# Performance work log

Measured on AMD Instinct MI355X. Metric: run time of the kernel, lower is better.

## Reference

```python
import jax, jax.numpy as jnp
import numpy as np

VAR_CXCY = 0.1   # SSD encoding variances
VAR_WH = 0.2
THRESH = 0.5     # match threshold from forward()
EPS = 1e-6


def point_form(p):
    """[P,4] (cx,cy,w,h) -> (x1,y1,x2,y2)."""
    return jnp.concatenate([p[..., :2] - p[..., 2:] / 2,
                            p[..., :2] + p[..., 2:] / 2], axis=-1)


def iou(a, b):
    """a: [N,4] xyxy, b: [P,4] xyxy -> [N,P] jaccard overlap."""
    lt = jnp.maximum(a[:, None, :2], b[None, :, :2])
    rb = jnp.minimum(a[:, None, 2:], b[None, :, 2:])
    wh = jnp.clip(rb - lt, 0.0)
    inter = wh[..., 0] * wh[..., 1]
    area_a = (a[:, 2] - a[:, 0]) * (a[:, 3] - a[:, 1])
    area_b = (b[:, 2] - b[:, 0]) * (b[:, 3] - b[:, 1])
    return inter / (area_a[:, None] + area_b[None, :] - inter + EPS)


def match_one(gt, labels, priors, priors_pt):
    """SSD match for a single image.
    gt: [N,4] xyxy, labels: [N] int, priors: [P,4] cxcywh, priors_pt: [P,4] xyxy.
    Returns loc targets [P,4] and conf targets [P] (0 = background).
    """
    ov = iou(gt, priors_pt)                       # [N,P]
    best_prior_idx = jnp.argmax(ov, axis=1)        # [N] best prior per gt
    best_truth_ov = jnp.max(ov, axis=0)            # [P]
    best_truth_idx = jnp.argmax(ov, axis=0)        # [P] best gt per prior
    n = gt.shape[0]
    # ensure every gt keeps its best prior
    best_truth_ov = best_truth_ov.at[best_prior_idx].set(2.0)
    best_truth_idx = best_truth_idx.at[best_prior_idx].set(jnp.arange(n))
    matches = gt[best_truth_idx]                   # [P,4]
    conf = labels[best_truth_idx] + 1              # shift so 0 = background
    conf = jnp.where(best_truth_ov < THRESH, 0, conf)
    # encode matched boxes relative to priors
    m_cxcy = (matches[:, :2] + matches[:, 2:]) * 0.5
    m_wh = jnp.clip(matches[:, 2:] - matches[:, :2], EPS)
    g_cxcy = (m_cxcy - priors[:, :2]) / (VAR_CXCY * priors[:, 2:])
    g_wh = jnp.log(m_wh / priors[:, 2:]) / VAR_WH
    return jnp.concatenate([g_cxcy, g_wh], axis=1), conf


def setup_inputs() -> dict:
    key = jax.random.key(0)
    k1, k2, k3, k4, k5 = jax.random.split(key, 5)
    B, N, P = 32, 100, 8732
    # ground-truth boxes: valid xyxy corners in [0,1]
    xy1 = jax.random.uniform(k1, (B, N, 2)) * 0.7
    wh = 0.05 + jax.random.uniform(k2, (B, N, 2)) * 0.25
    gt_boxes = jnp.concatenate([xy1, xy1 + wh], axis=-1).astype(jnp.float32)
    gt_labels = jax.random.randint(k3, (B, N), 0, 20)
    # priors: cxcywh
    p_cxcy = jax.random.uniform(k4, (P, 2))
    p_wh = 0.05 + jax.random.uniform(k5, (P, 2)) * 0.45
    priors = jnp.concatenate([p_cxcy, p_wh], axis=-1).astype(jnp.float32)
    return {"gt_boxes": gt_boxes, "gt_labels": gt_labels, "priors": priors}


def reference(gt_boxes, gt_labels, priors):
    priors_pt = point_form(priors)
    loc_t, conf_t = jax.vmap(
        lambda g, l: match_one(g, l, priors, priors_pt))(gt_boxes, gt_labels)
    return loc_t, conf_t
```

## Files before the change

### kernel.cpp

```cpp
#include <hip/hip_runtime.h>

#pragma clang fp contract(off)

#define BB 32
#define NN 100
#define PP 8732
#define NBX 35

template <bool USE_PART>
__global__ __launch_bounds__(256) void k_iou_pass(
    const float* __restrict__ gt,
    const float* __restrict__ priors,
    unsigned long long* __restrict__ red,
    unsigned char* __restrict__ m8)
{
    __shared__ float s_area[NN];
    __shared__ unsigned long long s_part[NN][5];

    const int b = blockIdx.y;
    const int t = threadIdx.x;
    const int p = blockIdx.x * 256 + t;
    const bool valid = p < PP;
    const int pc = valid ? p : (PP - 1);

    const float4* __restrict__ gtb =
        reinterpret_cast<const float4*>(gt) + b * NN;

    if (t < NN) {
        float4 g = gtb[t];
        s_area[t] = (g.z - g.x) * (g.w - g.y);
    }

    const float4 pr = reinterpret_cast<const float4*>(priors)[pc];
    const float px1 = pr.x - pr.z * 0.5f;
    const float py1 = pr.y - pr.w * 0.5f;
    const float px2 = pr.x + pr.z * 0.5f;
    const float py2 = pr.y + pr.w * 0.5f;
    const float area_b = (px2 - px1) * (py2 - py1);

    float best_ov = -1.0f;
    int best_j = 0;

    const int wbase = blockIdx.x * 256 + (t & ~63);
    const int wid = t >> 6;
    const bool lane0 = (t & 63) == 0;

    __syncthreads();

    #pragma unroll 4
    for (int j = 0; j < NN; ++j) {
        float4 g = gtb[j];
        float area_a = s_area[j];
        float ltx = fmaxf(g.x, px1), lty = fmaxf(g.y, py1);
        float rbx = fminf(g.z, px2), rby = fminf(g.w, py2);
        float w = fmaxf(rbx - ltx, 0.0f), h = fmaxf(rby - lty, 0.0f);
        float inter = w * h;
        float iou = inter / (area_a + area_b - inter + 1e-6f);

        if (iou > best_ov) { best_ov = iou; best_j = j; }

        float m = iou;
        m = fmaxf(m, __shfl_xor(m, 1));
        m = fmaxf(m, __shfl_xor(m, 2));
        m = fmaxf(m, __shfl_xor(m, 4));
        m = fmaxf(m, __shfl_xor(m, 8));
        m = fmaxf(m, __shfl_xor(m, 16));
        m = fmaxf(m, __shfl_xor(m, 32));
        unsigned long long win = __ballot(iou == m);
        int lmin = __ffsll((long long)win) - 1;
        if (lane0) {
            s_part[j][wid] =
                ((unsigned long long)__float_as_uint(m) << 32) |
                (unsigned int)(~(wbase + lmin));
        }
    }
    __syncthreads();

    if (t < NN) {
        unsigned long long best = s_part[t][0];
        #pragma unroll
        for (int w = 1; w < 4; ++w) {
            unsigned long long k = s_part[t][w];
            if (k > best) best = k;
        }
        if (USE_PART) {
            red[((size_t)b * NBX + blockIdx.x) * NN + t] = best;
        } else {
            atomicMax(&red[b * NN + t], best);
        }
    }
    if (valid) {
        m8[b * PP + p] =
            (unsigned char)(best_j | ((best_ov < 0.5f) ? 0x80 : 0));
    }
}

template <bool USE_PART>
__global__ __launch_bounds__(256) void k_encode(
    const float* __restrict__ gt,
    const int*   __restrict__ labels,
    const float* __restrict__ priors,
    const unsigned long long* __restrict__ red,
    const unsigned char* __restrict__ m8,
    float* __restrict__ loc_out,
    float* __restrict__ conf_out)
{
    __shared__ int s_forced[256];

    const int b = blockIdx.y;
    const int t = threadIdx.x;
    const int p = blockIdx.x * 256 + t;

    s_forced[t] = -1;
    __syncthreads();
    if (t < NN) {
        unsigned long long best;
        if (USE_PART) {
            const unsigned long long* q = red + (size_t)b * NBX * NN + t;
            best = q[0];
            #pragma unroll 5
            for (int bx = 1; bx < NBX; ++bx) {
                unsigned long long k = q[(size_t)bx * NN];
                if (k > best) best = k;
            }
        } else {
            best = red[b * NN + t];
        }
        int kp = (int)~(unsigned int)(best & 0xFFFFFFFFull);
        int lp = kp - blockIdx.x * 256;
        if ((unsigned)lp < 256u) atomicMax(&s_forced[lp], t);
    }
    __syncthreads();

    if (p >= PP) return;
    const int forced_j = s_forced[t];

    const unsigned char m = m8[b * PP + p];
    const int j    = (forced_j >= 0) ? forced_j : (m & 0x7f);
    const int lab  = labels[b * NN + j];
    const int conf = (forced_j < 0 && (m & 0x80)) ? 0 : (lab + 1);

    const float4 pr = reinterpret_cast<const float4*>(priors)[p];
    const float4 g  = reinterpret_cast<const float4*>(gt)[b * NN + j];
    const float mcx = (g.x + g.z) * 0.5f;
    const float mcy = (g.y + g.w) * 0.5f;
    const float mw  = fmaxf(g.z - g.x, 1e-6f);
    const float mh  = fmaxf(g.w - g.y, 1e-6f);
    const float gcx = (mcx - pr.x) / (0.1f * pr.z);
    const float gcy = (mcy - pr.y) / (0.1f * pr.w);
    const float gw  = logf(mw / pr.z) / 0.2f;
    const float gh  = logf(mh / pr.w) / 0.2f;

    reinterpret_cast<float4*>(loc_out)[b * PP + p] =
        make_float4(gcx, gcy, gw, gh);
    conf_out[b * PP + p] = (float)conf;
}

extern "C" void kernel_launch(void* const* d_in, const int* in_sizes, int n_in,
                              void* d_out, int out_size, void* d_ws, size_t ws_size,
                              hipStream_t stream) {
    const float* gt     = (const float*)d_in[0];
    const int*   labels = (const int*)  d_in[1];
    const float* priors = (const float*)d_in[2];

    float* loc  = (float*)d_out;
    float* conf = (float*)d_out + (size_t)BB * PP * 4;

    const size_t part_bytes = (size_t)BB * NBX * NN * 8;
    const size_t m8_bytes   = (size_t)BB * PP;
    dim3 grid(NBX, BB);

    if (ws_size >= part_bytes + m8_bytes) {
        unsigned long long* part = (unsigned long long*)d_ws;
        unsigned char* m8 = (unsigned char*)d_ws + part_bytes;
        k_iou_pass<true><<<grid, 256, 0, stream>>>(gt, priors, part, m8);
        k_encode<true><<<grid, 256, 0, stream>>>(gt, labels, priors, part,
                                                 m8, loc, conf);
    } else {
        unsigned long long* gkey = (unsigned long long*)d_ws;
        unsigned char* m8 = (unsigned char*)d_ws + (size_t)BB * NN * 8;
        hipMemsetAsync(gkey, 0, (size_t)BB * NN * 8, stream);
        k_iou_pass<false><<<grid, 256, 0, stream>>>(gt, priors, gkey, m8);
        k_encode<false><<<grid, 256, 0, stream>>>(gt, labels, priors, gkey,
                                                  m8, loc, conf);
    }
}
```

Measured before the change: 114.8 us.

## Split per-gt best-prior reduction into dedicated row blocks, drop cross-block partials

Instead of doing a wave-wide shuffle-max and ballot for every gt inside the per-prior IoU loop, the match kernel now adds extra blocks in which each wave owns one gt and scans all priors itself. It then reduces with 64-bit key shuffles and writes a single key per gt. This removes the per-iteration shuffle/ballot work and the partial-array pass in the encode kernel. The cost is that the IoU is computed twice, once per orientation, and a long serial loop of about 137 iterations per wave runs in the row blocks.

```diff
diff --git a/kernel.cpp b/kernel.cpp
--- a/kernel.cpp
+++ b/kernel.cpp
@@ -6,101 +6,101 @@
 #define NN 100
 #define PP 8732
 #define NBX 35
+#define NRB 25
 
-template <bool USE_PART>
-__global__ __launch_bounds__(256) void k_iou_pass(
+__global__ __launch_bounds__(256) void k_match(
     const float* __restrict__ gt,
     const float* __restrict__ priors,
-    unsigned long long* __restrict__ red,
+    unsigned long long* __restrict__ gkey,
     unsigned char* __restrict__ m8)
 {
     __shared__ float s_area[NN];
-    __shared__ unsigned long long s_part[NN][5];
 
     const int b = blockIdx.y;
     const int t = threadIdx.x;
-    const int p = blockIdx.x * 256 + t;
-    const bool valid = p < PP;
-    const int pc = valid ? p : (PP - 1);
-
     const float4* __restrict__ gtb =
         reinterpret_cast<const float4*>(gt) + b * NN;
 
-    if (t < NN) {
-        float4 g = gtb[t];
-        s_area[t] = (g.z - g.x) * (g.w - g.y);
-    }
+    if (blockIdx.x < NBX) {
+        const int p = blockIdx.x * 256 + t;
+        const bool valid = p < PP;
+        const int pc = valid ? p : (PP - 1);
 
-    const float4 pr = reinterpret_cast<const float4*>(priors)[pc];
-    const float px1 = pr.x - pr.z * 0.5f;
-    const float py1 = pr.y - pr.w * 0.5f;
-    const float px2 = pr.x + pr.z * 0.5f;
-    const float py2 = pr.y + pr.w * 0.5f;
-    const float area_b = (px2 - px1) * (py2 - py1);
+        if (t < NN) {
+            float4 g = gtb[t];
+            s_area[t] = (g.z - g.x) * (g.w - g.y);
+        }
 
-    float best_ov = -1.0f;
-    int best_j = 0;
+        const float4 pr = reinterpret_cast<const float4*>(priors)[pc];
+        const float px1 = pr.x - pr.z * 0.5f;
+        const float py1 = pr.y - pr.w * 0.5f;
+        const float px2 = pr.x + pr.z * 0.5f;
+        const float py2 = pr.y + pr.w * 0.5f;
+        const float area_b = (px2 - px1) * (py2 - py1);
 
-    const int wbase = blockIdx.x * 256 + (t & ~63);
-    const int wid = t >> 6;
-    const bool lane0 = (t & 63) == 0;
+        float best_ov = -1.0f;
+        int best_j = 0;
 
-    __syncthreads();
+        __syncthreads();
 
-    #pragma unroll 4
-    for (int j = 0; j < NN; ++j) {
-        float4 g = gtb[j];
-        float area_a = s_area[j];
-        float ltx = fmaxf(g.x, px1), lty = fmaxf(g.y, py1);
-        float rbx = fminf(g.z, px2), rby = fminf(g.w, py2);
-        float w = fmaxf(rbx - ltx, 0.0f), h = fmaxf(rby - lty, 0.0f);
-        float inter = w * h;
-        float iou = inter / (area_a + area_b - inter + 1e-6f);
+        #pragma unroll 4
+        for (int j = 0; j < NN; ++j) {
+            float4 g = gtb[j];
+            float area_a = s_area[j];
+            float ltx = fmaxf(g.x, px1), lty = fmaxf(g.y, py1);
+            float rbx = fminf(g.z, px2), rby = fminf(g.w, py2);
+            float w = fmaxf(rbx - ltx, 0.0f), h = fmaxf(rby - lty, 0.0f);
+            float inter = w * h;
+            float iou = inter / (area_a + area_b - inter + 1e-6f);
+            if (iou > best_ov) { best_ov = iou; best_j = j; }
+        }
 
-        if (iou > best_ov) { best_ov = iou; best_j = j; }
+        if (valid) {
+            m8[b * PP + p] =
+                (unsigned char)(best_j | ((best_ov < 0.5f) ? 0x80 : 0));
+        }
+    } else {
+        const int wid = t >> 6;
+        const int lane = t & 63;
+        const int j = (blockIdx.x - NBX) * 4 + wid;
 
-        float m = iou;
-        m = fmaxf(m, __shfl_xor(m, 1));
-        m = fmaxf(m, __shfl_xor(m, 2));
-        m = fmaxf(m, __shfl_xor(m, 4));
-        m = fmaxf(m, __shfl_xor(m, 8));
-        m = fmaxf(m, __shfl_xor(m, 16));
-        m = fmaxf(m, __shfl_xor(m, 32));
-        unsigned long long win = __ballot(iou == m);
-        int lmin = __ffsll((long long)win) - 1;
-        if (lane0) {
-            s_part[j][wid] =
-                ((unsigned long long)__float_as_uint(m) << 32) |
-                (unsigned int)(~(wbase + lmin));
+        const float4 g = gtb[j];
+        const float area_a = (g.z - g.x) * (g.w - g.y);
+
+        unsigned long long best = 0ull;
+
+        for (int p = lane; p < PP; p += 64) {
+            const float4 pr = reinterpret_cast<const float4*>(priors)[p];
+            const float px1 = pr.x - pr.z * 0.5f;
+            const float py1 = pr.y - pr.w * 0.5f;
+            const float px2 = pr.x + pr.z * 0.5f;
+            const float py2 = pr.y + pr.w * 0.5f;
+            const float area_b = (px2 - px1) * (py2 - py1);
+            float ltx = fmaxf(g.x, px1), lty = fmaxf(g.y, py1);
+            float rbx = fminf(g.z, px2), rby = fminf(g.w, py2);
+            float w = fmaxf(rbx - ltx, 0.0f), h = fmaxf(rby - lty, 0.0f);
+            float inter = w * h;
+            float iou = inter / (area_a + area_b - inter + 1e-6f);
+            unsigned long long key =
+                ((unsigned long long)__float_as_uint(iou) << 32) |
+                (unsigned int)(~p);
+            if (key > best) best = key;
         }
-    }
-    __syncthreads();
 
-    if (t < NN) {
-        unsigned long long best = s_part[t][0];
         #pragma unroll
-        for (int w = 1; w < 4; ++w) {
-            unsigned long long k = s_part[t][w];
-            if (k > best) best = k;
+        for (int d = 1; d < 64; d <<= 1) {
+            unsigned long long o = __shfl_xor(best, d);
+            if (o > best) best = o;
         }
-        if (USE_PART) {
-            red[((size_t)b * NBX + blockIdx.x) * NN + t] = best;
-        } else {
-            atomicMax(&red[b * NN + t], best);
-        }
-    }
-    if (valid) {
-        m8[b * PP + p] =
-            (unsigned char)(best_j | ((best_ov < 0.5f) ? 0x80 : 0));
+        if (lane == 0) gkey[b * NN + j] = best;
     }
 }
 
-template <bool USE_PART>
 __global__ __launch_bounds__(256) void k_encode(
     const float* __restrict__ gt,
     const int*   __restrict__ labels,
     const float* __restrict__ priors,
-    const unsigned long long* __restrict__ red,
+    const unsigned long long* __restrict__ gkey,
     const unsigned char* __restrict__ m8,
     float* __restrict__ loc_out,
     float* __restrict__ conf_out)
@@ -114,18 +114,7 @@
     s_forced[t] = -1;
     __syncthreads();
     if (t < NN) {
-        unsigned long long best;
-        if (USE_PART) {
-            const unsigned long long* q = red + (size_t)b * NBX * NN + t;
-            best = q[0];
-            #pragma unroll 5
-            for (int bx = 1; bx < NBX; ++bx) {
-                unsigned long long k = q[(size_t)bx * NN];
-                if (k > best) best = k;
-            }
-        } else {
-            best = red[b * NN + t];
-        }
+        unsigned long long best = gkey[b * NN + t];
         int kp = (int)~(unsigned int)(best & 0xFFFFFFFFull);
         int lp = kp - blockIdx.x * 256;
         if ((unsigned)lp < 256u) atomicMax(&s_forced[lp], t);
@@ -166,22 +155,13 @@
     float* loc  = (float*)d_out;
     float* conf = (float*)d_out + (size_t)BB * PP * 4;
 
-    const size_t part_bytes = (size_t)BB * NBX * NN * 8;
-    const size_t m8_bytes   = (size_t)BB * PP;
-    dim3 grid(NBX, BB);
+    unsigned long long* gkey = (unsigned long long*)d_ws;
+    unsigned char* m8 = (unsigned char*)d_ws + (size_t)BB * NN * 8;
 
-    if (ws_size >= part_bytes + m8_bytes) {
-        unsigned long long* part = (unsigned long long*)d_ws;
-        unsigned char* m8 = (unsigned char*)d_ws + part_bytes;
-        k_iou_pass<true><<<grid, 256, 0, stream>>>(gt, priors, part, m8);
-        k_encode<true><<<grid, 256, 0, stream>>>(gt, labels, priors, part,
-                                                 m8, loc, conf);
-    } else {
-        unsigned long long* gkey = (unsigned long long*)d_ws;
-        unsigned char* m8 = (unsigned char*)d_ws + (size_t)BB * NN * 8;
-        hipMemsetAsync(gkey, 0, (size_t)BB * NN * 8, stream);
-        k_iou_pass<false><<<grid, 256, 0, stream>>>(gt, priors, gkey, m8);
-        k_encode<false><<<grid, 256, 0, stream>>>(gt, labels, priors, gkey,
-                                                  m8, loc, conf);
-    }
+    dim3 grid_m(NBX + NRB, BB);
+    dim3 grid_e(NBX, BB);
+
+    k_match<<<grid_m, 256, 0, stream>>>(gt, priors, gkey, m8);
+    k_encode<<<grid_e, 256, 0, stream>>>(gt, labels, priors, gkey,
+                                         m8, loc, conf);
 }
```

New measurement: 120.7 us. 1.05x slower.
